# Performance work log

Measured on AMD Instinct MI355X. Metric: run time of the kernel, lower is better.

## Reference

```python
import jax, jax.numpy as jnp
import numpy as np

BATCH, IN_F, OUT_F, GRID_PLUS_ORDER = 8192, 1024, 1024, 8

def setup_inputs() -> dict:
    key = jax.random.key(0)
    k1, k2, k3 = jax.random.split(key, 3)
    x = jax.random.normal(k1, (BATCH, IN_F), dtype=jnp.float32)
    base_weight = jax.random.normal(k2, (OUT_F, IN_F), dtype=jnp.float32) * 0.03
    spline_weight = jax.random.normal(k3, (OUT_F, IN_F, GRID_PLUS_ORDER), dtype=jnp.float32) * 0.1
    return {"x": x, "base_weight": base_weight, "spline_weight": spline_weight}

def reference(x, base_weight, spline_weight):
    # base_output = F.linear(x, base_weight) -> x @ W_b^T
    base_output = x @ base_weight.T  # [B, out]
    # Original: sum_{i,g} silu(x)[b,i] * spline_weight[o,i,g]
    # The grid/order axis g is never contracted with x, so it collapses:
    # silu(x) @ spline_weight.sum(-1).T  -- identical math, no [O,B,I,G] blowup.
    w_spline = jnp.sum(spline_weight, axis=-1)  # [out, in]
    spline_output = jax.nn.silu(x) @ w_spline.T  # [B, out]
    return base_output + spline_output
```

## Files before the change

kernel.cpp:

```cpp
#include <hip/hip_runtime.h>
#include <hip/hip_bf16.h>


#define BATCH 8192
#define IN_F 1024
#define OUT_F 1024
#define KP 2048

typedef unsigned short ushort_t;
typedef __attribute__((ext_vector_type(8))) short short8;
typedef __attribute__((ext_vector_type(4))) float f32x4;

__device__ __forceinline__ ushort_t f2bf(float f) {
  union { float f; unsigned int u; } v;
  v.f = f;
  unsigned int u = v.u;
  u += 0x7fffu + ((u >> 16) & 1u);
  return (ushort_t)(u >> 16);
}

#define PREP_A_BLOCKS 4096
#define PREP_S_BLOCKS 1024
#define PREP_B_BLOCKS 1024
#define PREP_BLOCKS (PREP_A_BLOCKS + PREP_S_BLOCKS + PREP_B_BLOCKS)

__global__ __launch_bounds__(256) void prep_all(
    const float* __restrict__ x, const float* __restrict__ Wb,
    const float* __restrict__ Ws, ushort_t* __restrict__ Apack,
    ushort_t* __restrict__ Wpack) {
  const int blk = blockIdx.x;
  const int t = threadIdx.x;

  if (blk < PREP_A_BLOCKS) {
    const int idx = blk * 256 + t;
    const int b = idx >> 7;
    const int i = (idx & 127) << 3;
    const float4 x0 = *(const float4*)(x + ((size_t)b << 10) + i);
    const float4 x1 = *(const float4*)(x + ((size_t)b << 10) + i + 4);
    float xv[8] = {x0.x, x0.y, x0.z, x0.w, x1.x, x1.y, x1.z, x1.w};
    ushort_t vb[8], vs[8];
#pragma unroll
    for (int j = 0; j < 8; ++j) {
      vb[j] = f2bf(xv[j]);
      vs[j] = f2bf(xv[j] / (1.0f + __expf(-xv[j])));
    }
    ushort_t* row = Apack + ((size_t)b << 11);
    *(short8*)(row + i) = *(short8*)vb;
    *(short8*)(row + IN_F + i) = *(short8*)vs;
  } else if (blk < PREP_A_BLOCKS + PREP_S_BLOCKS) {
    const int idx = (blk - PREP_A_BLOCKS) * 256 + t;
    const int o = idx >> 8;
    const int i0 = (idx & 255) << 2;
    ushort_t vs[4];
#pragma unroll
    for (int j = 0; j < 4; ++j) {
      const float4* p = (const float4*)(Ws + ((((size_t)o << 10) + i0 + j) << 3));
      const float4 a = p[0];
      const float4 b = p[1];
      vs[j] = f2bf(((a.x + a.y) + (a.z + a.w)) + ((b.x + b.y) + (b.z + b.w)));
    }
    *(ushort4*)(Wpack + ((size_t)o << 11) + IN_F + i0) = *(ushort4*)vs;
  } else {
    const int idx = (blk - PREP_A_BLOCKS - PREP_S_BLOCKS) * 256 + t;
    const int o = idx >> 8;
    const int c = (idx & 255) << 2;
    const float4 w = *(const float4*)(Wb + ((size_t)o << 10) + c);
    ushort4 v;
    v.x = f2bf(w.x); v.y = f2bf(w.y); v.z = f2bf(w.z); v.w = f2bf(w.w);
    *(ushort4*)(Wpack + ((size_t)o << 11) + c) = v;
  }
}

#define BM 256
#define BN 128
#define GBK 64
#define NSTEP (KP / GBK)
#define A_US 16384
#define B_US 8192
#define BUF_US (A_US + B_US)
#define NBUF 3

typedef const __attribute__((address_space(1))) unsigned int gas_uint;
typedef __attribute__((address_space(3))) unsigned int las_uint;
#define ASYNC16(l, g) \
  __builtin_amdgcn_global_load_lds((gas_uint*)(g), (las_uint*)(l), 16, 0, 0)

__device__ __forceinline__ void stage_tile(const ushort_t* ga, const ushort_t* gb,
                                           ushort_t* la, ushort_t* lb,
                                           size_t rskip) {
  ASYNC16(la, ga);
  ASYNC16(la + 4096, ga + rskip);
  ASYNC16(la + 8192, ga + 2 * rskip);
  ASYNC16(la + 12288, ga + 3 * rskip);
  ASYNC16(lb, gb);
  ASYNC16(lb + 4096, gb + rskip);
}

__device__ __forceinline__ void mfma_step(const ushort_t* __restrict__ ab,
                                          const ushort_t* __restrict__ bb,
                                          const int (&aoff)[2][4],
                                          const int (&boff)[2][4],
                                          f32x4 (&acc)[4][4]) {
#pragma unroll
  for (int kk = 0; kk < 2; ++kk) {
    short8 af[4], bf[4];
#pragma unroll
    for (int i = 0; i < 4; ++i) af[i] = *(const short8*)(ab + aoff[kk][i]);
#pragma unroll
    for (int i = 0; i < 4; ++i) bf[i] = *(const short8*)(bb + boff[kk][i]);
    __builtin_amdgcn_s_setprio(1);
#pragma unroll
    for (int mi = 0; mi < 4; ++mi)
#pragma unroll
      for (int ni = 0; ni < 4; ++ni)
        acc[mi][ni] = __builtin_amdgcn_mfma_f32_16x16x32_bf16(
            af[mi], bf[ni], acc[mi][ni], 0, 0, 0);
    __builtin_amdgcn_s_setprio(0);
  }
}

__global__ __launch_bounds__(512, 2) void gemm_packed(
    const ushort_t* __restrict__ A,
    const ushort_t* __restrict__ W,
    float* __restrict__ C) {
  __shared__ __align__(16) ushort_t lds[NBUF * BUF_US];

  const int t = threadIdx.x;
  const int flat = blockIdx.x;
  const int xcd = flat & 7;
  const int local = flat >> 3;
  const int nt = local >> 2;
  const int mt = xcd * 4 + (local & 3);

  const int lane = t & 63;
  const int wave = t >> 6;
  const int wr = wave >> 1;
  const int wc = wave & 1;
  const int lr = lane & 15;
  const int lq = lane >> 4;

  const int srow = t >> 3;
  const int kc = (t & 7) ^ (srow & 7);
  const ushort_t* ga = A + (size_t)(mt * BM + srow) * KP + kc * 8;
  const ushort_t* gb = W + (size_t)(nt * BN + srow) * KP + kc * 8;
  const int ldst = t * 8;
  const size_t rskip = (size_t)64 * KP;

  int aoff[2][4], boff[2][4];
#pragma unroll
  for (int kk = 0; kk < 2; ++kk)
#pragma unroll
    for (int i = 0; i < 4; ++i) {
      const int arow = wr * 64 + i * 16 + lr;
      const int brow = wc * 64 + i * 16 + lr;
      const int ks = kk * 4 + lq;
      aoff[kk][i] = arow * 64 + ((ks ^ (arow & 7)) << 3);
      boff[kk][i] = brow * 64 + ((ks ^ (brow & 7)) << 3);
    }

  f32x4 acc[4][4];
#pragma unroll
  for (int mi = 0; mi < 4; ++mi)
#pragma unroll
    for (int ni = 0; ni < 4; ++ni) acc[mi][ni] = (f32x4){0.f, 0.f, 0.f, 0.f};

  stage_tile(ga, gb, lds + ldst, lds + A_US + ldst, rskip);
  stage_tile(ga + GBK, gb + GBK, lds + BUF_US + ldst, lds + BUF_US + A_US + ldst,
             rskip);
  asm volatile("s_waitcnt vmcnt(6)" ::: "memory");
  __builtin_amdgcn_s_barrier();
  __builtin_amdgcn_sched_barrier(0);

  int co = 0;
  int so = 2 * BUF_US;
  const ushort_t* gpa = ga + 2 * GBK;
  const ushort_t* gpb = gb + 2 * GBK;
#pragma unroll 3
  for (int s = 0; s < NSTEP - 2; ++s) {
    stage_tile(gpa, gpb, lds + so + ldst, lds + so + A_US + ldst, rskip);
    gpa += GBK;
    gpb += GBK;
    mfma_step(lds + co, lds + co + A_US, aoff, boff, acc);
    asm volatile("s_waitcnt vmcnt(6)" ::: "memory");
    __builtin_amdgcn_s_barrier();
    __builtin_amdgcn_sched_barrier(0);
    co += BUF_US; if (co == NBUF * BUF_US) co = 0;
    so += BUF_US; if (so == NBUF * BUF_US) so = 0;
  }
  mfma_step(lds + co, lds + co + A_US, aoff, boff, acc);
  asm volatile("s_waitcnt vmcnt(0)" ::: "memory");
  __builtin_amdgcn_s_barrier();
  __builtin_amdgcn_sched_barrier(0);
  co += BUF_US; if (co == NBUF * BUF_US) co = 0;
  mfma_step(lds + co, lds + co + A_US, aoff, boff, acc);

  const int col0 = nt * BN + wc * 64 + lr;
  const int row0 = mt * BM + wr * 64 + (lq << 2);
#pragma unroll
  for (int mi = 0; mi < 4; ++mi)
#pragma unroll
    for (int ni = 0; ni < 4; ++ni) {
      float* cp = C + (size_t)(row0 + mi * 16) * OUT_F + col0 + ni * 16;
#pragma unroll
      for (int rr = 0; rr < 4; ++rr) cp[(size_t)rr * OUT_F] = acc[mi][ni][rr];
    }
}

extern "C" void kernel_launch(void* const* d_in, const int* in_sizes, int n_in,
                              void* d_out, int out_size, void* d_ws, size_t ws_size,
                              hipStream_t stream) {
  const float* x = (const float*)d_in[0];
  const float* wb = (const float*)d_in[1];
  const float* ws = (const float*)d_in[2];
  float* out = (float*)d_out;

  ushort_t* Apack = (ushort_t*)d_ws;
  ushort_t* Wpack = (ushort_t*)((char*)d_ws + (size_t)BATCH * KP * 2);

  prep_all<<<PREP_BLOCKS, 256, 0, stream>>>(x, wb, ws, Apack, Wpack);
  gemm_packed<<<dim3((BATCH / BM) * (OUT_F / BN)), dim3(512), 0, stream>>>(Apack, Wpack, out);
}
```

Before: 143.6 us.

## Interleave LDS reads, async global loads and MFMA clusters in four phases

Splits each K-step of the GEMM main loop into four phases. Each phase issues a few LDS fragment reads and a pair of async global-to-LDS copies, then waits on lgkmcnt and runs an 8-MFMA cluster, with workgroup barriers between phases. The aim is to overlap memory traffic with matrix math in a fixed ping-pong schedule instead of one bulk load followed by all 32 MFMAs. It adds several extra s_barrier calls per step and forces strict waits, which could stall the waves if the phases are not balanced.

```diff
diff --git a/kernel.cpp b/kernel.cpp
--- a/kernel.cpp
+++ b/kernel.cpp
@@ -85,39 +85,10 @@
 #define ASYNC16(l, g) \
   __builtin_amdgcn_global_load_lds((gas_uint*)(g), (las_uint*)(l), 16, 0, 0)
 
-__device__ __forceinline__ void stage_tile(const ushort_t* ga, const ushort_t* gb,
-                                           ushort_t* la, ushort_t* lb,
-                                           size_t rskip) {
-  ASYNC16(la, ga);
-  ASYNC16(la + 4096, ga + rskip);
-  ASYNC16(la + 8192, ga + 2 * rskip);
-  ASYNC16(la + 12288, ga + 3 * rskip);
-  ASYNC16(lb, gb);
-  ASYNC16(lb + 4096, gb + rskip);
-}
-
-__device__ __forceinline__ void mfma_step(const ushort_t* __restrict__ ab,
-                                          const ushort_t* __restrict__ bb,
-                                          const int (&aoff)[2][4],
-                                          const int (&boff)[2][4],
-                                          f32x4 (&acc)[4][4]) {
-#pragma unroll
-  for (int kk = 0; kk < 2; ++kk) {
-    short8 af[4], bf[4];
-#pragma unroll
-    for (int i = 0; i < 4; ++i) af[i] = *(const short8*)(ab + aoff[kk][i]);
-#pragma unroll
-    for (int i = 0; i < 4; ++i) bf[i] = *(const short8*)(bb + boff[kk][i]);
-    __builtin_amdgcn_s_setprio(1);
-#pragma unroll
-    for (int mi = 0; mi < 4; ++mi)
-#pragma unroll
-      for (int ni = 0; ni < 4; ++ni)
-        acc[mi][ni] = __builtin_amdgcn_mfma_f32_16x16x32_bf16(
-            af[mi], bf[ni], acc[mi][ni], 0, 0, 0);
-    __builtin_amdgcn_s_setprio(0);
-  }
-}
+#define LGKM0() do { \
+  asm volatile("s_waitcnt lgkmcnt(0)" ::: "memory"); \
+  __builtin_amdgcn_sched_barrier(0); \
+} while (0)
 
 __global__ __launch_bounds__(512, 2) void gemm_packed(
     const ushort_t* __restrict__ A,
@@ -164,9 +135,17 @@
 #pragma unroll
     for (int ni = 0; ni < 4; ++ni) acc[mi][ni] = (f32x4){0.f, 0.f, 0.f, 0.f};
 
-  stage_tile(ga, gb, lds + ldst, lds + A_US + ldst, rskip);
-  stage_tile(ga + GBK, gb + GBK, lds + BUF_US + ldst, lds + BUF_US + A_US + ldst,
-             rskip);
+  {
+    ushort_t* la = lds + ldst;
+    ushort_t* lb = lds + A_US + ldst;
+    ASYNC16(la, ga);              ASYNC16(la + 4096, ga + rskip);
+    ASYNC16(la + 8192, ga + 2 * rskip); ASYNC16(la + 12288, ga + 3 * rskip);
+    ASYNC16(lb, gb);              ASYNC16(lb + 4096, gb + rskip);
+    la += BUF_US; lb += BUF_US;
+    ASYNC16(la, ga + GBK);              ASYNC16(la + 4096, ga + GBK + rskip);
+    ASYNC16(la + 8192, ga + GBK + 2 * rskip); ASYNC16(la + 12288, ga + GBK + 3 * rskip);
+    ASYNC16(lb, gb + GBK);              ASYNC16(lb + 4096, gb + GBK + rskip);
+  }
   asm volatile("s_waitcnt vmcnt(6)" ::: "memory");
   __builtin_amdgcn_s_barrier();
   __builtin_amdgcn_sched_barrier(0);
@@ -175,24 +154,102 @@
   int so = 2 * BUF_US;
   const ushort_t* gpa = ga + 2 * GBK;
   const ushort_t* gpb = gb + 2 * GBK;
+
+#define MFMA8(KK, N0)                                                        \
+  do {                                                                       \
+    __builtin_amdgcn_s_setprio(1);                                           \
+    _Pragma("unroll") for (int mi = 0; mi < 4; ++mi) {                       \
+      acc[mi][N0] = __builtin_amdgcn_mfma_f32_16x16x32_bf16(                 \
+          af##KK[mi], bf##KK[N0], acc[mi][N0], 0, 0, 0);                     \
+      acc[mi][N0 + 1] = __builtin_amdgcn_mfma_f32_16x16x32_bf16(             \
+          af##KK[mi], bf##KK[N0 + 1], acc[mi][N0 + 1], 0, 0, 0);             \
+    }                                                                        \
+    __builtin_amdgcn_s_setprio(0);                                           \
+  } while (0)
+
 #pragma unroll 3
   for (int s = 0; s < NSTEP - 2; ++s) {
-    stage_tile(gpa, gpb, lds + so + ldst, lds + so + A_US + ldst, rskip);
+    const ushort_t* ab = lds + co;
+    const ushort_t* bb = lds + co + A_US;
+    ushort_t* sa = lds + so + ldst;
+    ushort_t* sb = lds + so + A_US + ldst;
+    short8 af0[4], af1[4], bf0[4], bf1[4];
+
+#pragma unroll
+    for (int i = 0; i < 4; ++i) af0[i] = *(const short8*)(ab + aoff[0][i]);
+    bf0[0] = *(const short8*)(bb + boff[0][0]);
+    bf0[1] = *(const short8*)(bb + boff[0][1]);
+    ASYNC16(sa, gpa);
+    ASYNC16(sa + 4096, gpa + rskip);
+    __builtin_amdgcn_s_barrier();
+    LGKM0();
+    MFMA8(0, 0);
+    __builtin_amdgcn_s_barrier();
+
+    bf0[2] = *(const short8*)(bb + boff[0][2]);
+    bf0[3] = *(const short8*)(bb + boff[0][3]);
+    af1[0] = *(const short8*)(ab + aoff[1][0]);
+    af1[1] = *(const short8*)(ab + aoff[1][1]);
+    ASYNC16(sa + 8192, gpa + 2 * rskip);
+    ASYNC16(sa + 12288, gpa + 3 * rskip);
+    __builtin_amdgcn_s_barrier();
+    LGKM0();
+    MFMA8(0, 2);
+    __builtin_amdgcn_s_barrier();
+
+    af1[2] = *(const short8*)(ab + aoff[1][2]);
+    af1[3] = *(const short8*)(ab + aoff[1][3]);
+    bf1[0] = *(const short8*)(bb + boff[1][0]);
+    bf1[1] = *(const short8*)(bb + boff[1][1]);
+    ASYNC16(sb, gpb);
+    ASYNC16(sb + 4096, gpb + rskip);
+    __builtin_amdgcn_s_barrier();
+    LGKM0();
+    MFMA8(1, 0);
+    __builtin_amdgcn_s_barrier();
+
+    bf1[2] = *(const short8*)(bb + boff[1][2]);
+    bf1[3] = *(const short8*)(bb + boff[1][3]);
+    __builtin_amdgcn_s_barrier();
+    LGKM0();
+    MFMA8(1, 2);
+    asm volatile("s_waitcnt vmcnt(6)" ::: "memory");
+    __builtin_amdgcn_s_barrier();
+    __builtin_amdgcn_sched_barrier(0);
+
     gpa += GBK;
     gpb += GBK;
-    mfma_step(lds + co, lds + co + A_US, aoff, boff, acc);
-    asm volatile("s_waitcnt vmcnt(6)" ::: "memory");
-    __builtin_amdgcn_s_barrier();
-    __builtin_amdgcn_sched_barrier(0);
     co += BUF_US; if (co == NBUF * BUF_US) co = 0;
     so += BUF_US; if (so == NBUF * BUF_US) so = 0;
   }
-  mfma_step(lds + co, lds + co + A_US, aoff, boff, acc);
-  asm volatile("s_waitcnt vmcnt(0)" ::: "memory");
-  __builtin_amdgcn_s_barrier();
-  __builtin_amdgcn_sched_barrier(0);
-  co += BUF_US; if (co == NBUF * BUF_US) co = 0;
-  mfma_step(lds + co, lds + co + A_US, aoff, boff, acc);
+
+#pragma unroll 1
+  for (int s = 0; s < 2; ++s) {
+    const ushort_t* ab = lds + co;
+    const ushort_t* bb = lds + co + A_US;
+    short8 af0[4], af1[4], bf0[4], bf1[4];
+#pragma unroll
+    for (int kk = 0; kk < 2; ++kk) { (void)kk; }
+#pragma unroll
+    for (int i = 0; i < 4; ++i) af0[i] = *(const short8*)(ab + aoff[0][i]);
+#pragma unroll
+    for (int i = 0; i < 4; ++i) bf0[i] = *(const short8*)(bb + boff[0][i]);
+#pragma unroll
+    for (int i = 0; i < 4; ++i) af1[i] = *(const short8*)(ab + aoff[1][i]);
+#pragma unroll
+    for (int i = 0; i < 4; ++i) bf1[i] = *(const short8*)(bb + boff[1][i]);
+    LGKM0();
+    MFMA8(0, 0);
+    MFMA8(0, 2);
+    MFMA8(1, 0);
+    MFMA8(1, 2);
+    if (s == 0) {
+      asm volatile("s_waitcnt vmcnt(0)" ::: "memory");
+      __builtin_amdgcn_s_barrier();
+      __builtin_amdgcn_sched_barrier(0);
+      co += BUF_US; if (co == NBUF * BUF_US) co = 0;
+    }
+  }
 
   const int col0 = nt * BN + wc * 64 + lr;
   const int row0 = mt * BM + wr * 64 + (lq << 2);
```

Measured after the change: 140.8 us. 1.02x faster.

## Split-K GEMM with 256x256 tiles, 4-slot pipeline and atomic accumulation

Applied to the files above, without the earlier changes.

Replaces the 256x128 tile GEMM with 256x256 tiles and a 2-way split over K, giving 256 blocks that fit in one wave across the CUs. Partial sums are combined with float atomic adds into an output that the prep kernel now zeroes. The K loop uses 32-wide sub-steps, a 4-slot LDS ring, and A/B staging interleaved between two MFMA halves. The larger tile is meant to cut global and LDS traffic per FLOP. In exchange it adds atomic traffic, an output-zeroing pass and more barriers per step.

```diff
diff --git a/kernel.cpp b/kernel.cpp
--- a/kernel.cpp
+++ b/kernel.cpp
@@ -22,12 +22,13 @@
 #define PREP_A_BLOCKS 4096
 #define PREP_S_BLOCKS 1024
 #define PREP_B_BLOCKS 1024
-#define PREP_BLOCKS (PREP_A_BLOCKS + PREP_S_BLOCKS + PREP_B_BLOCKS)
+#define PREP_C_BLOCKS 2048
+#define PREP_BLOCKS (PREP_A_BLOCKS + PREP_S_BLOCKS + PREP_B_BLOCKS + PREP_C_BLOCKS)
 
 __global__ __launch_bounds__(256) void prep_all(
     const float* __restrict__ x, const float* __restrict__ Wb,
     const float* __restrict__ Ws, ushort_t* __restrict__ Apack,
-    ushort_t* __restrict__ Wpack) {
+    ushort_t* __restrict__ Wpack, float* __restrict__ Czero) {
   const int blk = blockIdx.x;
   const int t = threadIdx.x;
 
@@ -60,7 +61,7 @@
       vs[j] = f2bf(((a.x + a.y) + (a.z + a.w)) + ((b.x + b.y) + (b.z + b.w)));
     }
     *(ushort4*)(Wpack + ((size_t)o << 11) + IN_F + i0) = *(ushort4*)vs;
-  } else {
+  } else if (blk < PREP_A_BLOCKS + PREP_S_BLOCKS + PREP_B_BLOCKS) {
     const int idx = (blk - PREP_A_BLOCKS - PREP_S_BLOCKS) * 256 + t;
     const int o = idx >> 8;
     const int c = (idx & 255) << 2;
@@ -68,141 +69,154 @@
     ushort4 v;
     v.x = f2bf(w.x); v.y = f2bf(w.y); v.z = f2bf(w.z); v.w = f2bf(w.w);
     *(ushort4*)(Wpack + ((size_t)o << 11) + c) = v;
+  } else {
+    const int idx = blk - (PREP_A_BLOCKS + PREP_S_BLOCKS + PREP_B_BLOCKS);
+    float4* p = (float4*)Czero + (((size_t)(idx * 256 + t)) << 2);
+    const float4 z = make_float4(0.f, 0.f, 0.f, 0.f);
+    p[0] = z; p[1] = z; p[2] = z; p[3] = z;
   }
 }
 
 #define BM 256
-#define BN 128
-#define GBK 64
-#define NSTEP (KP / GBK)
-#define A_US 16384
-#define B_US 8192
-#define BUF_US (A_US + B_US)
-#define NBUF 3
+#define BN 256
+#define KHALF 1024
+#define SUBK 32
+#define NSUB (KHALF / SUBK)
+#define SLOT_A 8192
+#define SLOT_US 16384
+#define NSLOT 4
 
 typedef const __attribute__((address_space(1))) unsigned int gas_uint;
 typedef __attribute__((address_space(3))) unsigned int las_uint;
 #define ASYNC16(l, g) \
   __builtin_amdgcn_global_load_lds((gas_uint*)(g), (las_uint*)(l), 16, 0, 0)
 
-__device__ __forceinline__ void stage_tile(const ushort_t* ga, const ushort_t* gb,
-                                           ushort_t* la, ushort_t* lb,
-                                           size_t rskip) {
-  ASYNC16(la, ga);
-  ASYNC16(la + 4096, ga + rskip);
-  ASYNC16(la + 8192, ga + 2 * rskip);
-  ASYNC16(la + 12288, ga + 3 * rskip);
-  ASYNC16(lb, gb);
-  ASYNC16(lb + 4096, gb + rskip);
-}
-
-__device__ __forceinline__ void mfma_step(const ushort_t* __restrict__ ab,
-                                          const ushort_t* __restrict__ bb,
-                                          const int (&aoff)[2][4],
-                                          const int (&boff)[2][4],
-                                          f32x4 (&acc)[4][4]) {
-#pragma unroll
-  for (int kk = 0; kk < 2; ++kk) {
-    short8 af[4], bf[4];
-#pragma unroll
-    for (int i = 0; i < 4; ++i) af[i] = *(const short8*)(ab + aoff[kk][i]);
-#pragma unroll
-    for (int i = 0; i < 4; ++i) bf[i] = *(const short8*)(bb + boff[kk][i]);
-    __builtin_amdgcn_s_setprio(1);
-#pragma unroll
-    for (int mi = 0; mi < 4; ++mi)
-#pragma unroll
-      for (int ni = 0; ni < 4; ++ni)
-        acc[mi][ni] = __builtin_amdgcn_mfma_f32_16x16x32_bf16(
-            af[mi], bf[ni], acc[mi][ni], 0, 0, 0);
-    __builtin_amdgcn_s_setprio(0);
-  }
-}
-
-__global__ __launch_bounds__(512, 2) void gemm_packed(
+#define LGKM0() do { \
+  asm volatile("s_waitcnt lgkmcnt(0)" ::: "memory"); \
+  __builtin_amdgcn_sched_barrier(0); \
+} while (0)
+
+__global__ __launch_bounds__(512, 2) void gemm_splitk(
     const ushort_t* __restrict__ A,
     const ushort_t* __restrict__ W,
     float* __restrict__ C) {
-  __shared__ __align__(16) ushort_t lds[NBUF * BUF_US];
+  __shared__ __align__(16) ushort_t lds[NSLOT * SLOT_US];
 
   const int t = threadIdx.x;
   const int flat = blockIdx.x;
-  const int xcd = flat & 7;
-  const int local = flat >> 3;
-  const int nt = local >> 2;
-  const int mt = xcd * 4 + (local & 3);
+  const int ks = flat >> 7;
+  const int tile = flat & 127;
+  const int loc = tile & 31;
+  const int nt = tile >> 5;
+  const int mt = (loc & 7) * 4 + (loc >> 3);
 
   const int lane = t & 63;
   const int wave = t >> 6;
-  const int wr = wave >> 1;
-  const int wc = wave & 1;
+  const int wr = wave >> 2;
+  const int wc = wave & 3;
   const int lr = lane & 15;
   const int lq = lane >> 4;
 
-  const int srow = t >> 3;
-  const int kc = (t & 7) ^ (srow & 7);
-  const ushort_t* ga = A + (size_t)(mt * BM + srow) * KP + kc * 8;
-  const ushort_t* gb = W + (size_t)(nt * BN + srow) * KP + kc * 8;
+  const int srow = t >> 2;
+  const int sc = (t & 3) ^ (srow & 3);
+  const ushort_t* ga = A + (size_t)(mt * BM + srow) * KP + ks * KHALF + sc * 8;
+  const ushort_t* gb = W + (size_t)(nt * BN + srow) * KP + ks * KHALF + sc * 8;
+  const size_t rskip = (size_t)128 * KP;
   const int ldst = t * 8;
-  const size_t rskip = (size_t)64 * KP;
-
-  int aoff[2][4], boff[2][4];
-#pragma unroll
-  for (int kk = 0; kk < 2; ++kk)
-#pragma unroll
-    for (int i = 0; i < 4; ++i) {
-      const int arow = wr * 64 + i * 16 + lr;
-      const int brow = wc * 64 + i * 16 + lr;
-      const int ks = kk * 4 + lq;
-      aoff[kk][i] = arow * 64 + ((ks ^ (arow & 7)) << 3);
-      boff[kk][i] = brow * 64 + ((ks ^ (brow & 7)) << 3);
-    }
-
-  f32x4 acc[4][4];
-#pragma unroll
-  for (int mi = 0; mi < 4; ++mi)
+
+  int aoff[8], boff[4];
+#pragma unroll
+  for (int mi = 0; mi < 8; ++mi) {
+    const int arow = wr * 128 + mi * 16 + lr;
+    aoff[mi] = arow * 32 + ((lq ^ (arow & 3)) << 3);
+  }
+#pragma unroll
+  for (int ni = 0; ni < 4; ++ni) {
+    const int brow = wc * 64 + ni * 16 + lr;
+    boff[ni] = brow * 32 + ((lq ^ (brow & 3)) << 3);
+  }
+
+  f32x4 acc[8][4];
+#pragma unroll
+  for (int mi = 0; mi < 8; ++mi)
 #pragma unroll
     for (int ni = 0; ni < 4; ++ni) acc[mi][ni] = (f32x4){0.f, 0.f, 0.f, 0.f};
 
-  stage_tile(ga, gb, lds + ldst, lds + A_US + ldst, rskip);
-  stage_tile(ga + GBK, gb + GBK, lds + BUF_US + ldst, lds + BUF_US + A_US + ldst,
-             rskip);
-  asm volatile("s_waitcnt vmcnt(6)" ::: "memory");
+#define STAGE_A(slotoff, gka) do { \
+    ASYNC16(lds + (slotoff) + ldst, (gka)); \
+    ASYNC16(lds + (slotoff) + 4096 + ldst, (gka) + rskip); \
+  } while (0)
+#define STAGE_B(slotoff, gkb) do { \
+    ASYNC16(lds + (slotoff) + SLOT_A + ldst, (gkb)); \
+    ASYNC16(lds + (slotoff) + SLOT_A + 4096 + ldst, (gkb) + rskip); \
+  } while (0)
+
+#define MFMA16(MB)                                                           \
+  do {                                                                       \
+    __builtin_amdgcn_s_setprio(1);                                           \
+    _Pragma("unroll") for (int mi = 0; mi < 4; ++mi)                         \
+        _Pragma("unroll") for (int ni = 0; ni < 4; ++ni)                     \
+            acc[(MB) + mi][ni] = __builtin_amdgcn_mfma_f32_16x16x32_bf16(    \
+                af[mi], bf[ni], acc[(MB) + mi][ni], 0, 0, 0);                \
+    __builtin_amdgcn_s_setprio(0);                                           \
+  } while (0)
+
+  STAGE_A(0, ga);                    STAGE_B(0, gb);
+  STAGE_A(SLOT_US, ga + SUBK);       STAGE_B(SLOT_US, gb + SUBK);
+  STAGE_A(2 * SLOT_US, ga + 2 * SUBK); STAGE_B(2 * SLOT_US, gb + 2 * SUBK);
+  asm volatile("s_waitcnt vmcnt(8)" ::: "memory");
   __builtin_amdgcn_s_barrier();
   __builtin_amdgcn_sched_barrier(0);
 
-  int co = 0;
-  int so = 2 * BUF_US;
-  const ushort_t* gpa = ga + 2 * GBK;
-  const ushort_t* gpb = gb + 2 * GBK;
-#pragma unroll 3
-  for (int s = 0; s < NSTEP - 2; ++s) {
-    stage_tile(gpa, gpb, lds + so + ldst, lds + so + A_US + ldst, rskip);
-    gpa += GBK;
-    gpb += GBK;
-    mfma_step(lds + co, lds + co + A_US, aoff, boff, acc);
-    asm volatile("s_waitcnt vmcnt(6)" ::: "memory");
+#pragma unroll 4
+  for (int s = 0; s < NSUB; ++s) {
+    const ushort_t* ab = lds + (s & 3) * SLOT_US;
+    const ushort_t* bb = ab + SLOT_A;
+    const int so = ((s + 3) & 3) * SLOT_US;
+    const ushort_t* gpa = ga + (s + 3) * SUBK;
+    const ushort_t* gpb = gb + (s + 3) * SUBK;
+    short8 af[4], bf[4];
+
+#pragma unroll
+    for (int i = 0; i < 4; ++i) af[i] = *(const short8*)(ab + aoff[i]);
+#pragma unroll
+    for (int i = 0; i < 4; ++i) bf[i] = *(const short8*)(bb + boff[i]);
+    if (s < NSUB - 3) STAGE_A(so, gpa);
     __builtin_amdgcn_s_barrier();
+    LGKM0();
+    MFMA16(0);
+    __builtin_amdgcn_s_barrier();
+
+#pragma unroll
+    for (int i = 0; i < 4; ++i) af[i] = *(const short8*)(ab + aoff[4 + i]);
+    if (s < NSUB - 3) STAGE_B(so, gpb);
+    __builtin_amdgcn_s_barrier();
+    LGKM0();
+    MFMA16(4);
+    if (s < NSUB - 3) {
+      asm volatile("s_waitcnt vmcnt(8)" ::: "memory");
+    } else if (s == NSUB - 3) {
+      asm volatile("s_waitcnt vmcnt(4)" ::: "memory");
+    } else if (s == NSUB - 2) {
+      asm volatile("s_waitcnt vmcnt(0)" ::: "memory");
+    }
     __builtin_amdgcn_sched_barrier(0);
-    co += BUF_US; if (co == NBUF * BUF_US) co = 0;
-    so += BUF_US; if (so == NBUF * BUF_US) so = 0;
-  }
-  mfma_step(lds + co, lds + co + A_US, aoff, boff, acc);
-  asm volatile("s_waitcnt vmcnt(0)" ::: "memory");
-  __builtin_amdgcn_s_barrier();
-  __builtin_amdgcn_sched_barrier(0);
-  co += BUF_US; if (co == NBUF * BUF_US) co = 0;
-  mfma_step(lds + co, lds + co + A_US, aoff, boff, acc);
+    if (s < NSUB - 1) {
+      __builtin_amdgcn_s_barrier();
+      __builtin_amdgcn_sched_barrier(0);
+    }
+  }
 
   const int col0 = nt * BN + wc * 64 + lr;
-  const int row0 = mt * BM + wr * 64 + (lq << 2);
-#pragma unroll
-  for (int mi = 0; mi < 4; ++mi)
+  const int row0 = mt * BM + wr * 128 + (lq << 2);
+#pragma unroll
+  for (int mi = 0; mi < 8; ++mi)
 #pragma unroll
     for (int ni = 0; ni < 4; ++ni) {
       float* cp = C + (size_t)(row0 + mi * 16) * OUT_F + col0 + ni * 16;
 #pragma unroll
-      for (int rr = 0; rr < 4; ++rr) cp[(size_t)rr * OUT_F] = acc[mi][ni][rr];
+      for (int rr = 0; rr < 4; ++rr)
+        unsafeAtomicAdd(cp + (size_t)rr * OUT_F, acc[mi][ni][rr]);
     }
 }
 
@@ -217,6 +231,6 @@
   ushort_t* Apack = (ushort_t*)d_ws;
   ushort_t* Wpack = (ushort_t*)((char*)d_ws + (size_t)BATCH * KP * 2);
 
-  prep_all<<<PREP_BLOCKS, 256, 0, stream>>>(x, wb, ws, Apack, Wpack);
-  gemm_packed<<<dim3((BATCH / BM) * (OUT_F / BN)), dim3(512), 0, stream>>>(Apack, Wpack, out);
-}
+  prep_all<<<PREP_BLOCKS, 256, 0, stream>>>(x, wb, ws, Apack, Wpack, out);
+  gemm_splitk<<<dim3(256), dim3(512), 0, stream>>>(Apack, Wpack, out);
+}
```

New measurement: 194.5 us. +35.4%, slower.

## Load B fragments directly from global into registers, stage only A in LDS

Applied to the files above, without the earlier changes.

The weight (B) tile is no longer staged through LDS. Each wave loads its MFMA B fragments straight from global memory into double-buffered registers one step ahead, and only the A tile goes through the 3-slot async LDS pipeline. This cuts LDS footprint and traffic and drops the B LDS reads. The cost is redundant global B loads (the two wave rows sharing a column each fetch it), more VGPR pressure, and global latency exposed inside the MFMA loop.

```diff
diff --git a/kernel.cpp b/kernel.cpp
--- a/kernel.cpp
+++ b/kernel.cpp
@@ -75,55 +75,19 @@
 #define BN 128
 #define GBK 64
 #define NSTEP (KP / GBK)
-#define A_US 16384
-#define B_US 8192
-#define BUF_US (A_US + B_US)
-#define NBUF 3
+#define SLOT_US 16384
+#define NSLOT 3
 
 typedef const __attribute__((address_space(1))) unsigned int gas_uint;
 typedef __attribute__((address_space(3))) unsigned int las_uint;
 #define ASYNC16(l, g) \
   __builtin_amdgcn_global_load_lds((gas_uint*)(g), (las_uint*)(l), 16, 0, 0)
 
-__device__ __forceinline__ void stage_tile(const ushort_t* ga, const ushort_t* gb,
-                                           ushort_t* la, ushort_t* lb,
-                                           size_t rskip) {
-  ASYNC16(la, ga);
-  ASYNC16(la + 4096, ga + rskip);
-  ASYNC16(la + 8192, ga + 2 * rskip);
-  ASYNC16(la + 12288, ga + 3 * rskip);
-  ASYNC16(lb, gb);
-  ASYNC16(lb + 4096, gb + rskip);
-}
-
-__device__ __forceinline__ void mfma_step(const ushort_t* __restrict__ ab,
-                                          const ushort_t* __restrict__ bb,
-                                          const int (&aoff)[2][4],
-                                          const int (&boff)[2][4],
-                                          f32x4 (&acc)[4][4]) {
-#pragma unroll
-  for (int kk = 0; kk < 2; ++kk) {
-    short8 af[4], bf[4];
-#pragma unroll
-    for (int i = 0; i < 4; ++i) af[i] = *(const short8*)(ab + aoff[kk][i]);
-#pragma unroll
-    for (int i = 0; i < 4; ++i) bf[i] = *(const short8*)(bb + boff[kk][i]);
-    __builtin_amdgcn_s_setprio(1);
-#pragma unroll
-    for (int mi = 0; mi < 4; ++mi)
-#pragma unroll
-      for (int ni = 0; ni < 4; ++ni)
-        acc[mi][ni] = __builtin_amdgcn_mfma_f32_16x16x32_bf16(
-            af[mi], bf[ni], acc[mi][ni], 0, 0, 0);
-    __builtin_amdgcn_s_setprio(0);
-  }
-}
-
 __global__ __launch_bounds__(512, 2) void gemm_packed(
     const ushort_t* __restrict__ A,
     const ushort_t* __restrict__ W,
     float* __restrict__ C) {
-  __shared__ __align__(16) ushort_t lds[NBUF * BUF_US];
+  __shared__ __align__(16) ushort_t lds[NSLOT * SLOT_US];
 
   const int t = threadIdx.x;
   const int flat = blockIdx.x;
@@ -142,21 +106,26 @@
   const int srow = t >> 3;
   const int kc = (t & 7) ^ (srow & 7);
   const ushort_t* ga = A + (size_t)(mt * BM + srow) * KP + kc * 8;
-  const ushort_t* gb = W + (size_t)(nt * BN + srow) * KP + kc * 8;
   const int ldst = t * 8;
   const size_t rskip = (size_t)64 * KP;
 
-  int aoff[2][4], boff[2][4];
+  int aoff[2][4];
 #pragma unroll
   for (int kk = 0; kk < 2; ++kk)
 #pragma unroll
     for (int i = 0; i < 4; ++i) {
       const int arow = wr * 64 + i * 16 + lr;
-      const int brow = wc * 64 + i * 16 + lr;
       const int ks = kk * 4 + lq;
       aoff[kk][i] = arow * 64 + ((ks ^ (arow & 7)) << 3);
-      boff[kk][i] = brow * 64 + ((ks ^ (brow & 7)) << 3);
-    }
+    }
+
+  const ushort_t* bp[8];
+#pragma unroll
+  for (int j = 0; j < 8; ++j) {
+    const int ni = j & 3;
+    const int kk = j >> 2;
+    bp[j] = W + (size_t)(nt * BN + wc * 64 + ni * 16 + lr) * KP + kk * 32 + lq * 8;
+  }
 
   f32x4 acc[4][4];
 #pragma unroll
@@ -164,35 +133,93 @@
 #pragma unroll
     for (int ni = 0; ni < 4; ++ni) acc[mi][ni] = (f32x4){0.f, 0.f, 0.f, 0.f};
 
-  stage_tile(ga, gb, lds + ldst, lds + A_US + ldst, rskip);
-  stage_tile(ga + GBK, gb + GBK, lds + BUF_US + ldst, lds + BUF_US + A_US + ldst,
-             rskip);
-  asm volatile("s_waitcnt vmcnt(6)" ::: "memory");
+  short8 b0[8], b1[8];
+  int co = 0;
+  int so = 2 * SLOT_US;
+  const ushort_t* gsa = ga + 2 * GBK;
+  int gk = GBK;
+
+#define STAGE_A4()                                                            \
+  do {                                                                        \
+    ushort_t* sa = lds + so + ldst;                                           \
+    ASYNC16(sa, gsa);                                                         \
+    ASYNC16(sa + 4096, gsa + rskip);                                          \
+    ASYNC16(sa + 8192, gsa + 2 * rskip);                                      \
+    ASYNC16(sa + 12288, gsa + 3 * rskip);                                     \
+    gsa += GBK;                                                               \
+  } while (0)
+
+#define GEMM_STEP(BC, BN, DO_PREFETCH, DO_STAGE)                              \
+  do {                                                                        \
+    const ushort_t* ab = lds + co;                                            \
+    short8 af[4];                                                             \
+    _Pragma("unroll") for (int i = 0; i < 4; ++i)                             \
+        af[i] = *(const short8*)(ab + aoff[0][i]);                            \
+    if (DO_PREFETCH) {                                                        \
+      _Pragma("unroll") for (int j = 0; j < 4; ++j)                           \
+          BN[j] = *(const short8*)(bp[j] + gk);                               \
+    }                                                                         \
+    __builtin_amdgcn_sched_barrier(0);                                        \
+    __builtin_amdgcn_s_setprio(1);                                            \
+    _Pragma("unroll") for (int mi = 0; mi < 4; ++mi)                          \
+        _Pragma("unroll") for (int ni = 0; ni < 4; ++ni)                      \
+            acc[mi][ni] = __builtin_amdgcn_mfma_f32_16x16x32_bf16(            \
+                af[mi], BC[ni], acc[mi][ni], 0, 0, 0);                        \
+    __builtin_amdgcn_s_setprio(0);                                            \
+    _Pragma("unroll") for (int i = 0; i < 4; ++i)                             \
+        af[i] = *(const short8*)(ab + aoff[1][i]);                            \
+    if (DO_PREFETCH) {                                                        \
+      _Pragma("unroll") for (int j = 4; j < 8; ++j)                           \
+          BN[j] = *(const short8*)(bp[j] + gk);                               \
+      gk += GBK;                                                              \
+    }                                                                         \
+    if (DO_STAGE) STAGE_A4();                                                 \
+    __builtin_amdgcn_sched_barrier(0);                                        \
+    __builtin_amdgcn_s_setprio(1);                                            \
+    _Pragma("unroll") for (int mi = 0; mi < 4; ++mi)                          \
+        _Pragma("unroll") for (int ni = 0; ni < 4; ++ni)                      \
+            acc[mi][ni] = __builtin_amdgcn_mfma_f32_16x16x32_bf16(            \
+                af[mi], BC[4 + ni], acc[mi][ni], 0, 0, 0);                    \
+    __builtin_amdgcn_s_setprio(0);                                            \
+  } while (0)
+
+#define ENDSTEP(VMC)                                                          \
+  do {                                                                        \
+    asm volatile("s_waitcnt vmcnt(" #VMC ")" ::: "memory");                   \
+    __builtin_amdgcn_s_barrier();                                             \
+    __builtin_amdgcn_sched_barrier(0);                                        \
+    co += SLOT_US; if (co == NSLOT * SLOT_US) co = 0;                         \
+    so += SLOT_US; if (so == NSLOT * SLOT_US) so = 0;                         \
+  } while (0)
+
+  {
+    ushort_t* sa0 = lds + ldst;
+    ASYNC16(sa0, ga);
+    ASYNC16(sa0 + 4096, ga + rskip);
+    ASYNC16(sa0 + 8192, ga + 2 * rskip);
+    ASYNC16(sa0 + 12288, ga + 3 * rskip);
+#pragma unroll
+    for (int j = 0; j < 8; ++j) b0[j] = *(const short8*)(bp[j]);
+    ushort_t* sa1 = lds + SLOT_US + ldst;
+    ASYNC16(sa1, ga + GBK);
+    ASYNC16(sa1 + 4096, ga + GBK + rskip);
+    ASYNC16(sa1 + 8192, ga + GBK + 2 * rskip);
+    ASYNC16(sa1 + 12288, ga + GBK + 3 * rskip);
+  }
+  asm volatile("s_waitcnt vmcnt(4)" ::: "memory");
   __builtin_amdgcn_s_barrier();
   __builtin_amdgcn_sched_barrier(0);
 
-  int co = 0;
-  int so = 2 * BUF_US;
-  const ushort_t* gpa = ga + 2 * GBK;
-  const ushort_t* gpb = gb + 2 * GBK;
-#pragma unroll 3
-  for (int s = 0; s < NSTEP - 2; ++s) {
-    stage_tile(gpa, gpb, lds + so + ldst, lds + so + A_US + ldst, rskip);
-    gpa += GBK;
-    gpb += GBK;
-    mfma_step(lds + co, lds + co + A_US, aoff, boff, acc);
-    asm volatile("s_waitcnt vmcnt(6)" ::: "memory");
-    __builtin_amdgcn_s_barrier();
-    __builtin_amdgcn_sched_barrier(0);
-    co += BUF_US; if (co == NBUF * BUF_US) co = 0;
-    so += BUF_US; if (so == NBUF * BUF_US) so = 0;
-  }
-  mfma_step(lds + co, lds + co + A_US, aoff, boff, acc);
-  asm volatile("s_waitcnt vmcnt(0)" ::: "memory");
-  __builtin_amdgcn_s_barrier();
-  __builtin_amdgcn_sched_barrier(0);
-  co += BUF_US; if (co == NBUF * BUF_US) co = 0;
-  mfma_step(lds + co, lds + co + A_US, aoff, boff, acc);
+#pragma unroll 1
+  for (int s2 = 0; s2 < (NSTEP - 2) / 2; ++s2) {
+    GEMM_STEP(b0, b1, true, true);
+    ENDSTEP(4);
+    GEMM_STEP(b1, b0, true, true);
+    ENDSTEP(4);
+  }
+  GEMM_STEP(b0, b1, true, false);
+  ENDSTEP(0);
+  GEMM_STEP(b1, b0, false, false);
 
   const int col0 = nt * BN + wc * 64 + lr;
   const int row0 = mt * BM + wr * 64 + (lq << 2);
```

New measurement: 188.3 us. 1.31x slower.
